# Optimization experiments

Measured on AMD Instinct MI355X. Metric: run time of the kernel, lower is better.

The kernel has to match this reference:

```python
import jax, jax.numpy as jnp
import numpy as np

K = 3  # hardcoded in DRKNN.__init__


def setup_inputs() -> dict:
    key = jax.random.key(0)
    k1, k2, k3 = jax.random.split(key, 3)
    N, Q, A, B = 100000, 1024, 8, 16
    dataTensorX = jax.random.normal(k1, (N, A, B), dtype=jnp.float32)
    dataTensorY = jax.random.normal(k2, (N, 3), dtype=jnp.float32)
    inputTensor = jax.random.normal(k3, (Q, A, B), dtype=jnp.float32)
    return {"dataTensorX": dataTensorX, "dataTensorY": dataTensorY, "inputTensor": inputTensor}


def reference(dataTensorX, dataTensorY, inputTensor):
    # Flatten feature dims (1,2) -> single feature axis F = A*B
    N = dataTensorX.shape[0]
    Q = inputTensor.shape[0]
    X = dataTensorX.reshape(N, -1)   # [N, F]
    Qf = inputTensor.reshape(Q, -1)  # [Q, F]
    # squared L2 distance via expansion: ||q||^2 - 2 q.x + ||x||^2 -> [Q, N]
    x2 = jnp.sum(X * X, axis=-1)     # [N]
    q2 = jnp.sum(Qf * Qf, axis=-1)   # [Q]
    dists = q2[:, None] - 2.0 * (Qf @ X.T) + x2[None, :]  # [Q, N]
    # k smallest distances == k largest of negated distances
    _, idx = jax.lax.top_k(-dists, K)  # idx: [Q, K] int32
    outs = dataTensorY[idx]            # [Q, K, label_dim]
    out = jnp.mean(outs, axis=1)       # [Q, label_dim]
    return out, idx
```

## Files before the change

### kernel.cpp

```cpp
#include <hip/hip_runtime.h>

#define F       128
#define TILE    128
#define NCHUNKS 64
#define KSTEP   32
#define TOPK    3
#define NSUB_MAX 3200
#define DINF    (__builtin_inff())
#define IMAX    0x7fffffff

typedef short short8 __attribute__((ext_vector_type(8)));
typedef float f32x4  __attribute__((ext_vector_type(4)));

__device__ __forceinline__ ushort f2bf(float f) {
    uint u = __float_as_uint(f);
    uint r = (u + 0x7fffu + ((u >> 16) & 1u)) >> 16;
    return (ushort)r;
}

__device__ __forceinline__ bool lex_less(float d1, int i1, float d2, int i2) {
    return (d1 < d2) || (d1 == d2 && i1 < i2);
}

__device__ __forceinline__ int slotOf(int n, int g, int s) {
    int gg = g ^ ((n >> 2) & 3);
    int ss = s ^ (n & 3);
    return (n * 4 + gg) * 4 + ss;
}

__device__ __forceinline__ void loadRows(const ushort* __restrict__ src, uint4* v, int t) {
    const int n = t & 127, half = t >> 7;
    const uint4* s4 = reinterpret_cast<const uint4*>(src + (size_t)n * F + half * 64);
    #pragma unroll
    for (int c = 0; c < 8; c++) v[c] = s4[c];
}
__device__ __forceinline__ void writeLDS(const uint4* v, uint4* sX16, int t) {
    const int n = t & 127, half = t >> 7;
    const uint* u = reinterpret_cast<const uint*>(v);
    #pragma unroll
    for (int sp = 0; sp < 2; sp++)
        #pragma unroll
        for (int g = 0; g < 4; g++) {
            int c0 = sp * 4 + (g >> 1);
            int i0 = (g & 1) * 2;
            uint4 slot = make_uint4(u[c0 * 4 + i0], u[c0 * 4 + i0 + 1],
                                    u[(c0 + 2) * 4 + i0], u[(c0 + 2) * 4 + i0 + 1]);
            sX16[slotOf(n, g, half * 2 + sp)] = slot;
        }
}


__global__ void conv_kernel(const float* __restrict__ src, ushort* __restrict__ dst,
                            float* __restrict__ nrm, int rows, int rowsPad) {
    int row  = blockIdx.x * 4 + (threadIdx.x >> 6);
    int lane = threadIdx.x & 63;
    if (row >= rowsPad) return;
    if (row < rows) {
        float2 v = *reinterpret_cast<const float2*>(&src[(size_t)row * F + lane * 2]);
        ushort2 b; b.x = f2bf(v.x); b.y = f2bf(v.y);
        *reinterpret_cast<ushort2*>(&dst[(size_t)row * F + lane * 2]) = b;
        float s = v.x * v.x + v.y * v.y;
        #pragma unroll
        for (int m = 32; m >= 1; m >>= 1) s += __shfl_xor(s, m, 64);
        if (lane == 0) nrm[row] = s;
    } else {
        *reinterpret_cast<ushort2*>(&dst[(size_t)row * F + lane * 2]) = make_ushort2(0, 0);
        if (lane == 0) nrm[row] = DINF;
    }
}

__global__ __launch_bounds__(256) void knn_p1(
    const ushort* __restrict__ Xbf, const ushort* __restrict__ Qbf,
    const float* __restrict__ x2f, float* __restrict__ part,
    int NTILES, int NSUB)
{
    __shared__ uint4 sX16[2048];
    __shared__ float sx2[TILE];

    const int t   = threadIdx.x;
    const int w   = t >> 6;
    const int l   = t & 63;
    const int l15 = l & 15;
    const int g   = l >> 4;
    const int chunk = blockIdx.x;
    const int qbase = blockIdx.y * TILE;
    const int tile0 = (int)(((long)chunk * NTILES) >> 6);
    const int tile1 = (int)(((long)(chunk + 1) * NTILES) >> 6);

    {
        uint4 qv[8];
        loadRows(Qbf + (size_t)qbase * F, qv, t);
        writeLDS(qv, sX16, t);
    }
    __syncthreads();
    short8 qf[2][4];
    #pragma unroll
    for (int fqi = 0; fqi < 2; fqi++)
        #pragma unroll
        for (int s = 0; s < 4; s++) {
            int qn = w * 32 + fqi * 16 + l15;
            qf[fqi][s] = *reinterpret_cast<const short8*>(&sX16[slotOf(qn, g, s)]);
        }

    uint4 v[8];
    loadRows(Xbf + (size_t)tile0 * TILE * F, v, t);

    for (int tile = tile0; tile < tile1; tile++) {
        __syncthreads();
        writeLDS(v, sX16, t);
        if (t < 32)
            *reinterpret_cast<float4*>(&sx2[t * 4]) =
                *reinterpret_cast<const float4*>(&x2f[tile * TILE + t * 4]);
        if (tile + 1 < tile1)
            loadRows(Xbf + (size_t)(tile + 1) * TILE * F, v, t);
        __syncthreads();

        f32x4 acc[8][2];
        #pragma unroll
        for (int fm = 0; fm < 8; fm++)
            #pragma unroll
            for (int fqi = 0; fqi < 2; fqi++)
                acc[fm][fqi] = (f32x4){0.f, 0.f, 0.f, 0.f};

        #pragma unroll
        for (int s = 0; s < 4; s++) {
            short8 af[8];
            #pragma unroll
            for (int fm = 0; fm < 8; fm++)
                af[fm] = *reinterpret_cast<const short8*>(&sX16[slotOf(fm * 16 + l15, g, s)]);
            #pragma unroll
            for (int fm = 0; fm < 8; fm++) {
                acc[fm][0] = __builtin_amdgcn_mfma_f32_16x16x32_bf16(af[fm], qf[0][s], acc[fm][0], 0, 0, 0);
                acc[fm][1] = __builtin_amdgcn_mfma_f32_16x16x32_bf16(af[fm], qf[1][s], acc[fm][1], 0, 0, 0);
            }
        }

        #pragma unroll
        for (int sb = 0; sb < 4; sb++) {
            float4 xa = *reinterpret_cast<const float4*>(&sx2[sb * 32 + g * 4]);
            float4 xb = *reinterpret_cast<const float4*>(&sx2[sb * 32 + 16 + g * 4]);
            #pragma unroll
            for (int fqi = 0; fqi < 2; fqi++) {
                f32x4 ca = acc[sb * 2][fqi];
                f32x4 cb = acc[sb * 2 + 1][fqi];
                float t0 = fmaf(-2.f, ca[0], xa.x), t1 = fmaf(-2.f, ca[1], xa.y);
                float t2 = fmaf(-2.f, ca[2], xa.z), t3 = fmaf(-2.f, ca[3], xa.w);
                float t4 = fmaf(-2.f, cb[0], xb.x), t5 = fmaf(-2.f, cb[1], xb.y);
                float t6 = fmaf(-2.f, cb[2], xb.z), t7 = fmaf(-2.f, cb[3], xb.w);
                float m = fminf(fminf(fminf(t0, t1), fminf(t2, t3)),
                                fminf(fminf(t4, t5), fminf(t6, t7)));
                m = fminf(m, __shfl_xor(m, 16, 64));
                m = fminf(m, __shfl_xor(m, 32, 64));
                if (g == 0)
                    part[(size_t)(qbase + w * 32 + fqi * 16 + l15) * NSUB + (tile * 4 + sb)] = m;
            }
        }
    }
}

__global__ __launch_bounds__(256) void knn_p2(
    const float* __restrict__ part, const float* __restrict__ Xf,
    const float* __restrict__ x2f, const float* __restrict__ Qf,
    const float* __restrict__ q2f, const float* __restrict__ Y,
    float* __restrict__ out, int NSUB, int qTotal, int Nreal)
{
    __shared__ float spart[NSUB_MAX];
    __shared__ float sq[F];
    __shared__ float rd3[4][3];
    __shared__ int   scnt;
    __shared__ int   slist[256];
    __shared__ float wrd[4][3];
    __shared__ int   wri[4][3];

    const int t = threadIdx.x, w = t >> 6, l = t & 63;
    const int q = blockIdx.x;

    if (t < 64)
        *reinterpret_cast<float2*>(&sq[t * 2]) =
            *reinterpret_cast<const float2*>(&Qf[(size_t)q * F + t * 2]);
    if (t == 0) scnt = 0;

    const size_t prow = (size_t)q * NSUB;
    for (int i = t; i < NSUB; i += 256) spart[i] = part[prow + i];
    __syncthreads();

    float a0 = DINF, a1 = DINF, a2 = DINF;
    for (int i = t; i < NSUB; i += 256) {
        float v = spart[i];
        if (v < a2) { a2 = v;
            if (a2 < a1) { float x = a2; a2 = a1; a1 = x; }
            if (a1 < a0) { float x = a1; a1 = a0; a0 = x; } }
    }
    #pragma unroll
    for (int m = 1; m < 64; m <<= 1) {
        float o0 = __shfl_xor(a0, m, 64), o1 = __shfl_xor(a1, m, 64), o2 = __shfl_xor(a2, m, 64);
        #pragma unroll
        for (int c = 0; c < 3; c++) {
            float v = (c == 0) ? o0 : (c == 1) ? o1 : o2;
            if (v < a2) { a2 = v;
                if (a2 < a1) { float x = a2; a2 = a1; a1 = x; }
                if (a1 < a0) { float x = a1; a1 = a0; a0 = x; } }
        }
    }
    if (l == 0) { rd3[w][0] = a0; rd3[w][1] = a1; rd3[w][2] = a2; }
    __syncthreads();

    float tau;
    {
        float c0 = DINF, c1 = DINF, c2 = DINF;
        #pragma unroll
        for (int ww = 0; ww < 4; ww++)
            #pragma unroll
            for (int c = 0; c < 3; c++) {
                float v = rd3[ww][c];
                if (v < c2) { c2 = v;
                    if (c2 < c1) { float x = c2; c2 = c1; c1 = x; }
                    if (c1 < c0) { float x = c1; c1 = c0; c0 = x; } }
            }
        tau = c2 + 4.5f;
    }

    for (int i = t; i < NSUB; i += 256) {
        if (spart[i] <= tau) {
            int slot = atomicAdd(&scnt, 1);
            if (slot < 256) slist[slot] = i;
        }
    }
    __syncthreads();
    const int ncand = min(scnt, 256);
    const float q2v = q2f[q];

    float b0d = DINF, b1d = DINF, b2d = DINF;
    int   b0i = IMAX, b1i = IMAX, b2i = IMAX;
    auto ins = [&](float d, int ix) {
        if (lex_less(d, ix, b2d, b2i)) {
            b2d = d; b2i = ix;
            if (lex_less(b2d, b2i, b1d, b1i)) {
                float td = b2d; b2d = b1d; b1d = td; int ti = b2i; b2i = b1i; b1i = ti; }
            if (lex_less(b1d, b1i, b0d, b0i)) {
                float td = b1d; b1d = b0d; b0d = td; int ti = b1i; b1i = b0i; b0i = ti; }
        }
    };

    const int half = l >> 5, pl = l & 31;
    for (int ci = w; ci < ncand; ci += 4) {
        int p = slist[ci] * 32 + pl;
        float s = 0.f;
        if (p < Nreal) {
            const float4* xr = reinterpret_cast<const float4*>(&Xf[(size_t)p * F + half * 64]);
            const float4* qr = reinterpret_cast<const float4*>(&sq[half * 64]);
            float s0 = 0.f, s1 = 0.f, s2 = 0.f, s3 = 0.f;
            #pragma unroll
            for (int j = 0; j < 16; j++) {
                float4 xv = xr[j], qv = qr[j];
                s0 = fmaf(xv.x, qv.x, s0); s1 = fmaf(xv.y, qv.y, s1);
                s2 = fmaf(xv.z, qv.z, s2); s3 = fmaf(xv.w, qv.w, s3);
            }
            s = (s0 + s1) + (s2 + s3);
        }
        s += __shfl_xor(s, 32, 64);
        if (l < 32 && p < Nreal) {
            float d = (q2v - 2.0f * s) + x2f[p];
            ins(d, p);
        }
    }

    #pragma unroll
    for (int m = 1; m < 64; m <<= 1) {
        float od0 = __shfl_xor(b0d, m, 64); int oi0 = __shfl_xor(b0i, m, 64);
        float od1 = __shfl_xor(b1d, m, 64); int oi1 = __shfl_xor(b1i, m, 64);
        float od2 = __shfl_xor(b2d, m, 64); int oi2 = __shfl_xor(b2i, m, 64);
        ins(od0, oi0); ins(od1, oi1); ins(od2, oi2);
    }
    if (l == 0) {
        wrd[w][0] = b0d; wrd[w][1] = b1d; wrd[w][2] = b2d;
        wri[w][0] = b0i; wri[w][1] = b1i; wri[w][2] = b2i;
    }
    __syncthreads();

    if (t == 0) {
        #pragma unroll
        for (int ww = 1; ww < 4; ww++)
            #pragma unroll
            for (int c = 0; c < 3; c++)
                ins(wrd[ww][c], wri[ww][c]);
        int idx_off = qTotal * 3;
        #pragma unroll
        for (int c = 0; c < 3; c++) {
            float s = Y[(size_t)b0i * 3 + c] + Y[(size_t)b1i * 3 + c] + Y[(size_t)b2i * 3 + c];
            out[q * 3 + c] = s / 3.0f;
        }
        out[idx_off + q * 3 + 0] = (float)b0i;
        out[idx_off + q * 3 + 1] = (float)b1i;
        out[idx_off + q * 3 + 2] = (float)b2i;
    }
}


__global__ void fb_rownorm(const float* __restrict__ src, float* __restrict__ dst, int rows) {
    int row  = blockIdx.x * 4 + (threadIdx.x >> 6);
    int lane = threadIdx.x & 63;
    if (row >= rows) return;
    float2 v = *reinterpret_cast<const float2*>(&src[(size_t)row * F + lane * 2]);
    float s = v.x * v.x + v.y * v.y;
    #pragma unroll
    for (int m = 32; m >= 1; m >>= 1) s += __shfl_xor(s, m, 64);
    if (lane == 0) dst[row] = s;
}

__global__ __launch_bounds__(256) void fb_phase1(
    const float* __restrict__ X, const float* __restrict__ Qm,
    const float* __restrict__ x2, const float* __restrict__ q2,
    float* __restrict__ part_d, int* __restrict__ part_i,
    int N, int ntiles)
{
    __shared__ __align__(16) union {
        struct { float a[KSTEP * TILE]; float b[KSTEP * TILE]; } s;
        struct { float d[TILE][16][TOPK]; int i[TILE][16][TOPK]; } r;
    } u;

    const int t  = threadIdx.x;
    const int tx = t & 15;
    const int ty = t >> 4;
    const int chunk = blockIdx.x;
    const int qbase = blockIdx.y * TILE;
    const int ar0 = ty * 4;
    const int bc0 = tx * 4;
    const int srow0 = t >> 2;
    const int skc0  = t & 3;

    float t3d[8][TOPK];
    int   t3i[8][TOPK];
    #pragma unroll
    for (int i = 0; i < 8; i++)
        #pragma unroll
        for (int c = 0; c < TOPK; c++) { t3d[i][c] = DINF; t3i[i][c] = IMAX; }

    float q2r[8];
    #pragma unroll
    for (int i = 0; i < 8; i++) {
        int r = (i < 4) ? (ar0 + i) : (64 + ar0 + i - 4);
        q2r[i] = q2[qbase + r];
    }

    for (int tile = chunk; tile < ntiles; tile += NCHUNKS) {
        float acc[8][8];
        #pragma unroll
        for (int i = 0; i < 8; i++)
            #pragma unroll
            for (int j = 0; j < 8; j++) acc[i][j] = 0.0f;

        for (int ks = 0; ks < F; ks += KSTEP) {
            __syncthreads();
            #pragma unroll
            for (int lq = 0; lq < 4; lq++) {
                int row = srow0 | ((lq >> 1) << 6);
                int kc  = skc0 | ((lq & 1) << 2);
                int sw  = (kc & 3) << 3;
                int base = (kc * 4) * TILE + (row ^ sw);

                float4 va = *reinterpret_cast<const float4*>(
                    &Qm[(size_t)(qbase + row) * F + ks + kc * 4]);
                u.s.a[base + 0 * TILE] = va.x;
                u.s.a[base + 1 * TILE] = va.y;
                u.s.a[base + 2 * TILE] = va.z;
                u.s.a[base + 3 * TILE] = va.w;

                int n = tile * TILE + row;
                float4 vb = make_float4(0.f, 0.f, 0.f, 0.f);
                if (n < N) vb = *reinterpret_cast<const float4*>(
                    &X[(size_t)n * F + ks + kc * 4]);
                u.s.b[base + 0 * TILE] = vb.x;
                u.s.b[base + 1 * TILE] = vb.y;
                u.s.b[base + 2 * TILE] = vb.z;
                u.s.b[base + 3 * TILE] = vb.w;
            }
            __syncthreads();

            #pragma unroll
            for (int kk = 0; kk < KSTEP; kk++) {
                int sw = ((kk >> 2) & 3) << 3;
                float4 a0 = *reinterpret_cast<const float4*>(&u.s.a[kk * TILE + (ar0 ^ sw)]);
                float4 a1 = *reinterpret_cast<const float4*>(&u.s.a[kk * TILE + 64 + (ar0 ^ sw)]);
                float4 b0 = *reinterpret_cast<const float4*>(&u.s.b[kk * TILE + (bc0 ^ sw)]);
                float4 b1 = *reinterpret_cast<const float4*>(&u.s.b[kk * TILE + 64 + (bc0 ^ sw)]);
                float av[8] = {a0.x, a0.y, a0.z, a0.w, a1.x, a1.y, a1.z, a1.w};
                float bv[8] = {b0.x, b0.y, b0.z, b0.w, b1.x, b1.y, b1.z, b1.w};
                #pragma unroll
                for (int i = 0; i < 8; i++)
                    #pragma unroll
                    for (int j = 0; j < 8; j++)
                        acc[i][j] = fmaf(av[i], bv[j], acc[i][j]);
            }
        }

        #pragma unroll
        for (int j = 0; j < 8; j++) {
            int n = tile * TILE + ((j < 4) ? (bc0 + j) : (64 + bc0 + j - 4));
            if (n < N) {
                float xc = x2[n];
                #pragma unroll
                for (int i = 0; i < 8; i++) {
                    float d = (q2r[i] - 2.0f * acc[i][j]) + xc;
                    if (d < t3d[i][2]) {
                        t3d[i][2] = d; t3i[i][2] = n;
                        if (t3d[i][2] < t3d[i][1]) {
                            float td = t3d[i][2]; t3d[i][2] = t3d[i][1]; t3d[i][1] = td;
                            int ti = t3i[i][2]; t3i[i][2] = t3i[i][1]; t3i[i][1] = ti;
                        }
                        if (t3d[i][1] < t3d[i][0]) {
                            float td = t3d[i][1]; t3d[i][1] = t3d[i][0]; t3d[i][0] = td;
                            int ti = t3i[i][1]; t3i[i][1] = t3i[i][0]; t3i[i][0] = ti;
                        }
                    }
                }
            }
        }
    }

    __syncthreads();
    #pragma unroll
    for (int i = 0; i < 8; i++) {
        int r = (i < 4) ? (ar0 + i) : (64 + ar0 + i - 4);
        #pragma unroll
        for (int c = 0; c < TOPK; c++) {
            u.r.d[r][tx][c] = t3d[i][c];
            u.r.i[r][tx][c] = t3i[i][c];
        }
    }
    __syncthreads();

    if (t < TILE) {
        int row = t;
        float b0d = DINF, b1d = DINF, b2d = DINF;
        int   b0i = IMAX, b1i = IMAX, b2i = IMAX;
        for (int s = 0; s < 16; s++) {
            #pragma unroll
            for (int c = 0; c < TOPK; c++) {
                float d = u.r.d[row][s][c];
                int  ix = u.r.i[row][s][c];
                if (lex_less(d, ix, b2d, b2i)) {
                    b2d = d; b2i = ix;
                    if (lex_less(b2d, b2i, b1d, b1i)) {
                        float td = b2d; b2d = b1d; b1d = td;
                        int ti = b2i; b2i = b1i; b1i = ti;
                    }
                    if (lex_less(b1d, b1i, b0d, b0i)) {
                        float td = b1d; b1d = b0d; b0d = td;
                        int ti = b1i; b1i = b0i; b0i = ti;
                    }
                }
            }
        }
        size_t base = ((size_t)(qbase + row) * NCHUNKS + chunk) * TOPK;
        part_d[base + 0] = b0d; part_d[base + 1] = b1d; part_d[base + 2] = b2d;
        part_i[base + 0] = b0i; part_i[base + 1] = b1i; part_i[base + 2] = b2i;
    }
}

__global__ void fb_phase2(const float* __restrict__ part_d, const int* __restrict__ part_i,
                          const float* __restrict__ Y, float* __restrict__ out, int Q)
{
    int q    = blockIdx.x * 4 + (threadIdx.x >> 6);
    int lane = threadIdx.x & 63;
    if (q >= Q) return;

    float b0d = DINF, b1d = DINF, b2d = DINF;
    int   b0i = IMAX, b1i = IMAX, b2i = IMAX;

    auto ins = [&](float d, int ix) {
        if (lex_less(d, ix, b2d, b2i)) {
            b2d = d; b2i = ix;
            if (lex_less(b2d, b2i, b1d, b1i)) {
                float td = b2d; b2d = b1d; b1d = td;
                int ti = b2i; b2i = b1i; b1i = ti;
            }
            if (lex_less(b1d, b1i, b0d, b0i)) {
                float td = b1d; b1d = b0d; b0d = td;
                int ti = b1i; b1i = b0i; b0i = ti;
            }
        }
    };

    const int total = NCHUNKS * TOPK;
    size_t base = (size_t)q * total;
    for (int e = lane; e < total; e += 64)
        ins(part_d[base + e], part_i[base + e]);

    #pragma unroll
    for (int m = 1; m < 64; m <<= 1) {
        float od0 = __shfl_xor(b0d, m, 64); int oi0 = __shfl_xor(b0i, m, 64);
        float od1 = __shfl_xor(b1d, m, 64); int oi1 = __shfl_xor(b1i, m, 64);
        float od2 = __shfl_xor(b2d, m, 64); int oi2 = __shfl_xor(b2i, m, 64);
        ins(od0, oi0); ins(od1, oi1); ins(od2, oi2);
    }

    if (lane == 0) {
        int idx_off = Q * 3;
        #pragma unroll
        for (int c = 0; c < 3; c++) {
            float s = Y[(size_t)b0i * 3 + c] + Y[(size_t)b1i * 3 + c] + Y[(size_t)b2i * 3 + c];
            out[q * 3 + c] = s / 3.0f;
        }
        out[idx_off + q * 3 + 0] = (float)b0i;
        out[idx_off + q * 3 + 1] = (float)b1i;
        out[idx_off + q * 3 + 2] = (float)b2i;
    }
}


extern "C" void kernel_launch(void* const* d_in, const int* in_sizes, int n_in,
                              void* d_out, int out_size, void* d_ws, size_t ws_size,
                              hipStream_t stream) {
    const float* Xf = (const float*)d_in[0];
    const float* Y  = (const float*)d_in[1];
    const float* Qf = (const float*)d_in[2];
    int N = in_sizes[1] / 3;
    int Q = in_sizes[2] / F;
    int NTILES = (N + TILE - 1) / TILE;
    int NPAD   = NTILES * TILE;
    int NSUB   = NTILES * 4;
    char* ws = (char*)d_ws;
    (void)n_in; (void)out_size;

    size_t oA = 0;
    auto allocA = [&](size_t b) { size_t r = oA; oA = (oA + b + 255) & ~(size_t)255; return r; };
    size_t off_Xbf  = allocA((size_t)NPAD * F * 2);
    size_t off_Qbf  = allocA((size_t)Q * F * 2);
    size_t off_x2   = allocA((size_t)NPAD * 4);
    size_t off_q2   = allocA((size_t)Q * 4);
    size_t off_part = allocA((size_t)NSUB * Q * 4);

    if (oA <= ws_size && NSUB <= NSUB_MAX) {
        ushort* Xbf  = (ushort*)(ws + off_Xbf);
        ushort* Qbf  = (ushort*)(ws + off_Qbf);
        float*  x2f  = (float*) (ws + off_x2);
        float*  q2f  = (float*) (ws + off_q2);
        float*  part = (float*) (ws + off_part);

        hipLaunchKernelGGL(conv_kernel, dim3(NPAD / 4), dim3(256), 0, stream, Xf, Xbf, x2f, N, NPAD);
        hipLaunchKernelGGL(conv_kernel, dim3(Q / 4),    dim3(256), 0, stream, Qf, Qbf, q2f, Q, Q);
        hipLaunchKernelGGL(knn_p1, dim3(NCHUNKS, Q / TILE), dim3(256), 0, stream,
                           Xbf, Qbf, x2f, part, NTILES, NSUB);
        hipLaunchKernelGGL(knn_p2, dim3(Q), dim3(256), 0, stream,
                           part, Xf, x2f, Qf, q2f, Y, (float*)d_out, NSUB, Q, N);
    } else {
        size_t oB = 0;
        auto allocB = [&](size_t b) { size_t r = oB; oB = (oB + b + 255) & ~(size_t)255; return r; };
        float* x2     = (float*)(ws + allocB((size_t)N * 4));
        float* q2     = (float*)(ws + allocB((size_t)Q * 4));
        float* part_d = (float*)(ws + allocB((size_t)Q * NCHUNKS * TOPK * 4));
        int*   part_i = (int*)  (ws + allocB((size_t)Q * NCHUNKS * TOPK * 4));

        hipLaunchKernelGGL(fb_rownorm, dim3((N + 3) / 4), dim3(256), 0, stream, Xf, x2, N);
        hipLaunchKernelGGL(fb_rownorm, dim3((Q + 3) / 4), dim3(256), 0, stream, Qf, q2, Q);
        hipLaunchKernelGGL(fb_phase1, dim3(NCHUNKS, Q / TILE), dim3(256), 0, stream,
                           Xf, Qf, x2, q2, part_d, part_i, N, NTILES);
        hipLaunchKernelGGL(fb_phase2, dim3((Q + 3) / 4), dim3(256), 0, stream,
                           part_d, part_i, Y, (float*)d_out, Q);
    }
}
```

Before: 116.9 us.

## Double-buffer X tiles in LDS and remap waves to data rows

The knn_p1 GEMM kernel now keeps two LDS buffers for X tiles. The next tile is written while the current one is computed, so each tile needs one barrier instead of two. Each wave now owns 32 data rows against all 128 queries held in registers, rather than 32 queries against all 128 rows. That cuts per-wave LDS fragment reads but raises register pressure, since qf grows to 8x4 short8 and there are 16 accumulators. x2 norms are read straight from global memory instead of being staged in LDS, and launch bounds request 2 blocks per CU.

Result: slower. 171.8 us (+46.9%).

```diff
diff --git a/kernel.cpp b/kernel.cpp
--- a/kernel.cpp
+++ b/kernel.cpp
@@ -2,6 +2,8 @@
 
 #define F       128
 #define TILE    128
+#define QBLK    128
+#define FQI     8
 #define NCHUNKS 64
 #define KSTEP   32
 #define TOPK    3
@@ -69,13 +71,12 @@
     }
 }
 
-__global__ __launch_bounds__(256) void knn_p1(
+__global__ __launch_bounds__(256, 2) void knn_p1(
     const ushort* __restrict__ Xbf, const ushort* __restrict__ Qbf,
     const float* __restrict__ x2f, float* __restrict__ part,
     int NTILES, int NSUB)
 {
-    __shared__ uint4 sX16[2048];
-    __shared__ float sx2[TILE];
+    __shared__ uint4 sbuf[2][2048];
 
     const int t   = threadIdx.x;
     const int w   = t >> 6;
@@ -83,78 +84,75 @@
     const int l15 = l & 15;
     const int g   = l >> 4;
     const int chunk = blockIdx.x;
-    const int qbase = blockIdx.y * TILE;
+    const int qbase = blockIdx.y * QBLK;
     const int tile0 = (int)(((long)chunk * NTILES) >> 6);
     const int tile1 = (int)(((long)(chunk + 1) * NTILES) >> 6);
 
-    {
-        uint4 qv[8];
-        loadRows(Qbf + (size_t)qbase * F, qv, t);
-        writeLDS(qv, sX16, t);
-    }
-    __syncthreads();
-    short8 qf[2][4];
-    #pragma unroll
-    for (int fqi = 0; fqi < 2; fqi++)
+    uint4 v[8];
+
+    loadRows(Qbf + (size_t)qbase * F, v, t);
+    writeLDS(v, sbuf[0], t);
+    __syncthreads();
+    short8 qf[FQI][4];
+    #pragma unroll
+    for (int fqi = 0; fqi < FQI; fqi++)
+        #pragma unroll
+        for (int s = 0; s < 4; s++)
+            qf[fqi][s] = *reinterpret_cast<const short8*>(&sbuf[0][slotOf(fqi * 16 + l15, g, s)]);
+
+    loadRows(Xbf + (size_t)tile0 * TILE * F, v, t);
+    __syncthreads();
+    writeLDS(v, sbuf[0], t);
+    if (tile0 + 1 < tile1)
+        loadRows(Xbf + (size_t)(tile0 + 1) * TILE * F, v, t);
+    __syncthreads();
+
+    for (int i = 0; ; ) {
+        const int tile = tile0 + i;
+        const int cb = i & 1;
+
+        if (tile + 1 < tile1) {
+            writeLDS(v, sbuf[cb ^ 1], t);
+            if (tile + 2 < tile1)
+                loadRows(Xbf + (size_t)(tile + 2) * TILE * F, v, t);
+        }
+
+        f32x4 acc[2][FQI];
+        #pragma unroll
+        for (int fm = 0; fm < 2; fm++)
+            #pragma unroll
+            for (int fqi = 0; fqi < FQI; fqi++)
+                acc[fm][fqi] = (f32x4){0.f, 0.f, 0.f, 0.f};
+
         #pragma unroll
         for (int s = 0; s < 4; s++) {
-            int qn = w * 32 + fqi * 16 + l15;
-            qf[fqi][s] = *reinterpret_cast<const short8*>(&sX16[slotOf(qn, g, s)]);
-        }
-
-    uint4 v[8];
-    loadRows(Xbf + (size_t)tile0 * TILE * F, v, t);
-
-    for (int tile = tile0; tile < tile1; tile++) {
+            short8 af0 = *reinterpret_cast<const short8*>(&sbuf[cb][slotOf(w * 32 + l15, g, s)]);
+            short8 af1 = *reinterpret_cast<const short8*>(&sbuf[cb][slotOf(w * 32 + 16 + l15, g, s)]);
+            #pragma unroll
+            for (int fqi = 0; fqi < FQI; fqi++) {
+                acc[0][fqi] = __builtin_amdgcn_mfma_f32_16x16x32_bf16(af0, qf[fqi][s], acc[0][fqi], 0, 0, 0);
+                acc[1][fqi] = __builtin_amdgcn_mfma_f32_16x16x32_bf16(af1, qf[fqi][s], acc[1][fqi], 0, 0, 0);
+            }
+        }
+
+        float4 xv0 = *reinterpret_cast<const float4*>(&x2f[(size_t)tile * TILE + w * 32 + g * 4]);
+        float4 xv1 = *reinterpret_cast<const float4*>(&x2f[(size_t)tile * TILE + w * 32 + 16 + g * 4]);
+        #pragma unroll
+        for (int fqi = 0; fqi < FQI; fqi++) {
+            f32x4 a0 = acc[0][fqi];
+            f32x4 a1 = acc[1][fqi];
+            float m = fminf(fminf(fminf(fmaf(-2.f, a0[0], xv0.x), fmaf(-2.f, a0[1], xv0.y)),
+                                  fminf(fmaf(-2.f, a0[2], xv0.z), fmaf(-2.f, a0[3], xv0.w))),
+                            fminf(fminf(fmaf(-2.f, a1[0], xv1.x), fmaf(-2.f, a1[1], xv1.y)),
+                                  fminf(fmaf(-2.f, a1[2], xv1.z), fmaf(-2.f, a1[3], xv1.w))));
+            m = fminf(m, __shfl_xor(m, 16, 64));
+            m = fminf(m, __shfl_xor(m, 32, 64));
+            if (g == 0)
+                part[(size_t)(qbase + fqi * 16 + l15) * NSUB + (tile * 4 + w)] = m;
+        }
+
+        if (++i; tile0 + i >= tile1) break;
         __syncthreads();
-        writeLDS(v, sX16, t);
-        if (t < 32)
-            *reinterpret_cast<float4*>(&sx2[t * 4]) =
-                *reinterpret_cast<const float4*>(&x2f[tile * TILE + t * 4]);
-        if (tile + 1 < tile1)
-            loadRows(Xbf + (size_t)(tile + 1) * TILE * F, v, t);
-        __syncthreads();
-
-        f32x4 acc[8][2];
-        #pragma unroll
-        for (int fm = 0; fm < 8; fm++)
-            #pragma unroll
-            for (int fqi = 0; fqi < 2; fqi++)
-                acc[fm][fqi] = (f32x4){0.f, 0.f, 0.f, 0.f};
-
-        #pragma unroll
-        for (int s = 0; s < 4; s++) {
-            short8 af[8];
-            #pragma unroll
-            for (int fm = 0; fm < 8; fm++)
-                af[fm] = *reinterpret_cast<const short8*>(&sX16[slotOf(fm * 16 + l15, g, s)]);
-            #pragma unroll
-            for (int fm = 0; fm < 8; fm++) {
-                acc[fm][0] = __builtin_amdgcn_mfma_f32_16x16x32_bf16(af[fm], qf[0][s], acc[fm][0], 0, 0, 0);
-                acc[fm][1] = __builtin_amdgcn_mfma_f32_16x16x32_bf16(af[fm], qf[1][s], acc[fm][1], 0, 0, 0);
-            }
-        }
-
-        #pragma unroll
-        for (int sb = 0; sb < 4; sb++) {
-            float4 xa = *reinterpret_cast<const float4*>(&sx2[sb * 32 + g * 4]);
-            float4 xb = *reinterpret_cast<const float4*>(&sx2[sb * 32 + 16 + g * 4]);
-            #pragma unroll
-            for (int fqi = 0; fqi < 2; fqi++) {
-                f32x4 ca = acc[sb * 2][fqi];
-                f32x4 cb = acc[sb * 2 + 1][fqi];
-                float t0 = fmaf(-2.f, ca[0], xa.x), t1 = fmaf(-2.f, ca[1], xa.y);
-                float t2 = fmaf(-2.f, ca[2], xa.z), t3 = fmaf(-2.f, ca[3], xa.w);
-                float t4 = fmaf(-2.f, cb[0], xb.x), t5 = fmaf(-2.f, cb[1], xb.y);
-                float t6 = fmaf(-2.f, cb[2], xb.z), t7 = fmaf(-2.f, cb[3], xb.w);
-                float m = fminf(fminf(fminf(t0, t1), fminf(t2, t3)),
-                                fminf(fminf(t4, t5), fminf(t6, t7)));
-                m = fminf(m, __shfl_xor(m, 16, 64));
-                m = fminf(m, __shfl_xor(m, 32, 64));
-                if (g == 0)
-                    part[(size_t)(qbase + w * 32 + fqi * 16 + l15) * NSUB + (tile * 4 + sb)] = m;
-            }
-        }
     }
 }
 
@@ -531,7 +529,7 @@
     size_t off_q2   = allocA((size_t)Q * 4);
     size_t off_part = allocA((size_t)NSUB * Q * 4);
 
-    if (oA <= ws_size && NSUB <= NSUB_MAX) {
+    if (oA <= ws_size && NSUB <= NSUB_MAX && (Q % QBLK) == 0) {
         ushort* Xbf  = (ushort*)(ws + off_Xbf);
         ushort* Qbf  = (ushort*)(ws + off_Qbf);
         float*  x2f  = (float*) (ws + off_x2);
@@ -540,7 +538,7 @@
 
         hipLaunchKernelGGL(conv_kernel, dim3(NPAD / 4), dim3(256), 0, stream, Xf, Xbf, x2f, N, NPAD);
         hipLaunchKernelGGL(conv_kernel, dim3(Q / 4),    dim3(256), 0, stream, Qf, Qbf, q2f, Q, Q);
-        hipLaunchKernelGGL(knn_p1, dim3(NCHUNKS, Q / TILE), dim3(256), 0, stream,
+        hipLaunchKernelGGL(knn_p1, dim3(NCHUNKS, Q / QBLK), dim3(256), 0, stream,
                            Xbf, Qbf, x2f, part, NTILES, NSUB);
         hipLaunchKernelGGL(knn_p2, dim3(Q), dim3(256), 0, stream,
                            part, Xf, x2f, Qf, q2f, Y, (float*)d_out, NSUB, Q, N);
```
